# Optimization experiments

Hardware: AMD Instinct MI355X
Metric: run time of the kernel (lower is better)

## Reference

```python
import jax, jax.numpy as jnp
import numpy as np

B, W_DIM, CIN, COUT, K, H = 16, 512, 512, 512, 3, 64
PAD = (K - 1) // 2          # conv padding, also filtered_lrelu padding
GAIN = float(np.sqrt(2.0))  # lrelu gain (not torgb)
SLOPE = 0.2                 # lrelu slope (not torgb)
CLAMP = 256.0               # conv_clamp
AFFINE_WG = float(1.0 / np.sqrt(W_DIM))  # FullyConnectedLayer weight_gain


def setup_inputs() -> dict:
    key = jax.random.key(0)
    k0, k1, k2, k3 = jax.random.split(key, 4)
    return {
        "x": jax.random.normal(k0, (B, CIN, H, H), jnp.float32),
        "w": jax.random.normal(k1, (B, W_DIM), jnp.float32),
        "affine_weight": jax.random.normal(k2, (CIN, W_DIM), jnp.float32),
        "affine_bias": jnp.ones((CIN,), jnp.float32),       # bias_init=1
        "conv_weight": jax.random.normal(k3, (COUT, CIN, K, K), jnp.float32),
        "bias": jnp.zeros((COUT,), jnp.float32),
        "magnitude_ema": jnp.ones((), jnp.float32),
    }


def reference(x, w, affine_weight, affine_bias, conv_weight, bias, magnitude_ema):
    input_gain = jax.lax.rsqrt(magnitude_ema)
    # --- affine (FullyConnectedLayer, linear act, lr_mult=1) ---
    s = w @ (affine_weight * AFFINE_WG).T + affine_bias          # [B, CIN]
    # --- modulated_conv2d with demodulation (is_torgb=False) ---
    wk = conv_weight * jax.lax.rsqrt(
        jnp.mean(jnp.square(conv_weight), axis=(1, 2, 3), keepdims=True))
    s = s * jax.lax.rsqrt(jnp.mean(jnp.square(s)))
    wb = wk[None] * s[:, None, :, None, None]                    # [B,COUT,CIN,K,K]
    dcoefs = jax.lax.rsqrt(jnp.sum(jnp.square(wb), axis=(2, 3, 4)) + 1e-8)  # [B,COUT]
    wb = wb * dcoefs[:, :, None, None, None] * input_gain
    # grouped conv: groups = batch, one weight set per sample
    xg = x.reshape(1, B * CIN, H, H)
    wg = wb.reshape(B * COUT, CIN, K, K)
    y = jax.lax.conv_general_dilated(
        xg, wg, window_strides=(1, 1), padding=[(PAD, PAD), (PAD, PAD)],
        dimension_numbers=("NCHW", "OIHW", "NCHW"), feature_group_count=B)
    y = y.reshape(B, COUT, H, H)
    # --- filtered_lrelu: up=down=1, fu=fd=None (identity FIR) ---
    # => bias add, zero-pad by `padding`, lrelu * gain, clamp
    y = y + bias[:, None, None]
    y = jnp.pad(y, ((0, 0), (0, 0), (PAD, PAD), (PAD, PAD)))
    y = jnp.where(y >= 0, y, y * SLOPE) * GAIN
    y = jnp.clip(y, -CLAMP, CLAMP)                               # [B,COUT,66,66]
    return y
```

## Files before the change

kernel.cpp:

```cpp
#include <hip/hip_runtime.h>

#define B_     16
#define WDIM   512
#define CIN_   512
#define COUT_  512
#define HH     64
#define KC     32
#define NCHUNK (CIN_/KC)
#define AFFINE_WG 0.044194173824159216f
#define GAIN_  1.4142135623730951f
#define CLAMP_ 256.0f

typedef __attribute__((ext_vector_type(4))) float f32x4;
typedef __attribute__((ext_vector_type(8))) short bf16x8;
typedef __attribute__((ext_vector_type(8))) unsigned short u16x8;

__device__ __forceinline__ unsigned short f2bf(float f) {
    union { float f; unsigned u; } un; un.f = f;
    unsigned u = un.u;
    u += 0x7FFFu + ((u >> 16) & 1u);
    return (unsigned short)(u >> 16);
}

__device__ __forceinline__ void gl_lds16(const void* g, void* l) {
    __builtin_amdgcn_global_load_lds(
        reinterpret_cast<const __attribute__((address_space(1))) unsigned int*>(
            reinterpret_cast<uintptr_t>(g)),
        reinterpret_cast<__attribute__((address_space(3))) unsigned int*>(
            reinterpret_cast<uintptr_t>(l)),
        16, 0, 0);
}

__global__ void k_prepA(const float* __restrict__ w, const float* __restrict__ aw,
                        const float* __restrict__ ab, const float* __restrict__ cw,
                        float* __restrict__ s, float* __restrict__ part,
                        float* __restrict__ alpha, float* __restrict__ Q,
                        unsigned short* __restrict__ wb) {
    const int bi  = blockIdx.x;
    const int tid = threadIdx.x;
    __shared__ float redA[256];
    __shared__ float qsh[512];
    __shared__ float a_sh;
    __shared__ char tile[36864];

    if (bi < 32) {
        const int b = bi >> 1;
        const int c = ((bi & 1) << 8) + tid;
        const f32x4* wr = (const f32x4*)(w + (size_t)b * WDIM);
        const f32x4* ar = (const f32x4*)(aw + (size_t)c * WDIM);
        float acc = 0.f;
        #pragma unroll 4
        for (int k = 0; k < WDIM / 4; ++k) {
            f32x4 a = ar[k], bb = wr[k];
            acc += a[0]*bb[0] + a[1]*bb[1] + a[2]*bb[2] + a[3]*bb[3];
        }
        float sv = acc * AFFINE_WG + ab[c];
        s[b * CIN_ + c] = sv;
        redA[tid] = sv * sv;
        __syncthreads();
        for (int off = 128; off > 0; off >>= 1) {
            if (tid < off) redA[tid] += redA[tid + off];
            __syncthreads();
        }
        if (tid == 0) part[bi] = redA[0];
    } else if (bi < 544) {
        const int o = bi - 32;
        float tot = 0.f;
        #pragma unroll
        for (int half = 0; half < 2; ++half) {
            const int c = tid + half * 256;
            const float* p = cw + ((size_t)o * 512 + c) * 9;
            float qs = 0.f;
            #pragma unroll
            for (int t = 0; t < 9; ++t) { float v = p[t]; qs += v * v; }
            qsh[c] = qs; tot += qs;
        }
        redA[tid] = tot; __syncthreads();
        for (int off = 128; off > 0; off >>= 1) {
            if (tid < off) redA[tid] += redA[tid + off];
            __syncthreads();
        }
        if (tid == 0) { a_sh = rsqrtf(redA[0] * (1.0f / 4608.0f)); alpha[o] = a_sh; }
        __syncthreads();
        const float a2 = a_sh * a_sh;
        Q[(size_t)o * 512 + tid]       = a2 * qsh[tid];
        Q[(size_t)o * 512 + tid + 256] = a2 * qsh[tid + 256];
    } else {
        const int p = bi - 544;
        const int ot = p >> 4, cc = p & 15;
        const float* base = cw + ((size_t)(ot * 64) * 512 + cc * 32) * 9;
        #pragma unroll
        for (int k = 0; k < 18; ++k) {
            const int lin4 = tid + k * 256;
            const int row  = lin4 / 72;
            const int i4   = lin4 - row * 72;
            const f32x4 v = *(const f32x4*)(base + (size_t)row * 4608 + i4 * 4);
            #pragma unroll
            for (int j = 0; j < 4; ++j) {
                const int e   = i4 * 4 + j;
                const int c   = e / 9;
                const int tap = e - c * 9;
                const int byte = ((tap * 2048 + row * 32 + c) << 1) ^ ((row & 6) << 3);
                *(unsigned short*)(tile + byte) = f2bf(v[j]);
            }
        }
        __syncthreads();
        u16x8* dst = (u16x8*)(wb + (size_t)p * 18432);
        const u16x8* src = (const u16x8*)tile;
        #pragma unroll
        for (int k = 0; k < 9; ++k) dst[tid + k * 256] = src[tid + k * 256];
    }
}

__global__ void k_prepB(const float* __restrict__ x, const float* __restrict__ s,
                        const float* __restrict__ part, const float* __restrict__ Q,
                        const float* __restrict__ alpha, const float* __restrict__ ema,
                        float* __restrict__ g, unsigned short* __restrict__ xbf) {
    const int bi  = blockIdx.x;
    const int tid = threadIdx.x;
    __shared__ float rs2_sh;
    __shared__ char tile[8 * 4096];

    if (bi < 32) {
        const int b = bi >> 1;
        const int o = ((bi & 1) << 8) + tid;
        if (tid == 0) {
            float t = 0.f;
            #pragma unroll
            for (int i = 0; i < 32; ++i) t += part[i];
            rs2_sh = 8192.0f / t;
        }
        __syncthreads();
        const f32x4* sh = (const f32x4*)(s + (size_t)b * CIN_);
        const f32x4* qq = (const f32x4*)(Q + (size_t)o * CIN_);
        float d = 0.f;
        #pragma unroll 4
        for (int k = 0; k < CIN_ / 4; ++k) {
            f32x4 a = sh[k], q4 = qq[k];
            d += a[0]*a[0]*q4[0] + a[1]*a[1]*q4[1] + a[2]*a[2]*q4[2] + a[3]*a[3]*q4[3];
        }
        const float ig = rsqrtf(ema[0]);
        g[b * COUT_ + o] = alpha[o] * rsqrtf(d * rs2_sh + 1e-8f) * ig;
    } else {
        if (tid == 0) {
            float t = 0.f;
            #pragma unroll
            for (int i = 0; i < 32; ++i) t += part[i];
            rs2_sh = rsqrtf(t * (1.0f / 8192.0f));
        }
        __syncthreads();
        const float rs = rs2_sh;
        const int blk = bi - 32;
        const int b  = blk >> 7;
        const int cc = (blk >> 3) & 15;
        const int rg = blk & 7;
        const int c   = tid >> 3;
        const int k8  = tid & 7;
        const float sc = s[b * CIN_ + cc * 32 + c] * rs;
        const float* src = x + (((size_t)(b * CIN_ + cc * 32 + c)) * HH + rg * 8) * HH + k8 * 8;
        #pragma unroll
        for (int row = 0; row < 8; ++row) {
            const f32x4 v0 = *(const f32x4*)(src + (size_t)row * HH);
            const f32x4 v1 = *(const f32x4*)(src + (size_t)row * HH + 4);
            #pragma unroll
            for (int q = 0; q < 8; ++q) {
                const float v = (q < 4) ? v0[q] : v1[q - 4];
                const int col = k8 * 8 + q + 1;
                const int byte = ((col * 64 + 2 * c) ^ ((col & 6) << 3)) - 64;
                *(unsigned short*)(tile + row * 4096 + byte) = f2bf(v * sc);
            }
        }
        __syncthreads();
        unsigned short* dst = xbf + ((size_t)(b * 16 + cc) * 64 + rg * 8) * 2048;
        const u16x8* tsrc = (const u16x8*)tile;
        #pragma unroll
        for (int k = 0; k < 8; ++k)
            *(u16x8*)(dst + (size_t)(tid + k * 256) * 8) = tsrc[tid + k * 256];
    }
}

__global__ __launch_bounds__(256, 2) void k_conv2c(
    const unsigned short* __restrict__ xbf, const unsigned short* __restrict__ wb,
    const float* __restrict__ g, const float* __restrict__ bias,
    float* __restrict__ out) {
    __shared__ unsigned short Wlds[9 * 64 * 32];
    __shared__ unsigned short Xlds[6 * 66 * 32];

    const int tid  = threadIdx.x;
    const int lane = tid & 63;
    const int wv   = tid >> 6;
    const int l15  = lane & 15;
    const int hi   = lane >> 4;
    const int b  = blockIdx.z;
    const int ot = blockIdx.y;
    const int rt = blockIdx.x;
    const int h0 = rt * 4;

    const f32x4 zero4 = {0.f, 0.f, 0.f, 0.f};
    f32x4 acc[4][4];
    #pragma unroll
    for (int i = 0; i < 4; ++i)
        #pragma unroll
        for (int j = 0; j < 4; ++j) acc[i][j] = zero4;

    {
        unsigned int* p = (unsigned int*)Xlds;
        for (int i = tid; i < 6 * 66 * 32 / 2; i += 256) p[i] = 0u;
    }
    __syncthreads();

    const char* wsrc0 = (const char*)wb + (size_t)ot * 16 * 36864;
    const char* xsrc0 = (const char*)xbf + (size_t)b * 16 * 262144;

    for (int cc = 0; cc < NCHUNK; ++cc) {
        const char* wsrc = wsrc0 + (size_t)cc * 36864;
        #pragma unroll
        for (int r = 0; r < 9; ++r)
            gl_lds16(wsrc + r * 4096 + tid * 16,
                     (char*)Wlds + r * 4096 + wv * 1024);
        const char* xsrc = xsrc0 + (size_t)cc * 262144;
        #pragma unroll
        for (int r = 0; r < 6; ++r) {
            const int h_in = h0 - 1 + r;
            if ((unsigned)h_in < 64u)
                gl_lds16(xsrc + (size_t)h_in * 4096 + tid * 16,
                         (char*)Xlds + r * 4224 + 64 + wv * 1024);
        }
        __syncthreads();

        #pragma unroll
        for (int tap = 0; tap < 9; ++tap) {
            const int ti = tap / 3, tj = tap - ti * 3;
            bf16x8 af[4];
            #pragma unroll
            for (int mi = 0; mi < 4; ++mi) {
                const int o = mi * 16 + l15;
                int byte = (tap << 12) + (o << 6) + (hi << 4);
                byte ^= ((o & 6) << 3);
                af[mi] = *(const bf16x8*)((const char*)Wlds + byte);
            }
            bf16x8 bg[4];
            const int row = wv + ti;
            #pragma unroll
            for (int ni = 0; ni < 4; ++ni) {
                const int col = ni * 16 + l15 + tj;
                int byte = (((row * 66 + col) << 5) + (hi << 3)) << 1;
                byte ^= ((col & 6) << 3);
                bg[ni] = *(const bf16x8*)((const char*)Xlds + byte);
            }
            #pragma unroll
            for (int mi = 0; mi < 4; ++mi)
                #pragma unroll
                for (int ni = 0; ni < 4; ++ni)
                    acc[mi][ni] = __builtin_amdgcn_mfma_f32_16x16x32_bf16(
                        af[mi], bg[ni], acc[mi][ni], 0, 0, 0);
        }
        if (cc != NCHUNK - 1) __syncthreads();
    }

    {
        const int obase = ot * 64;
        const int orow = h0 + wv + 1;
        #pragma unroll
        for (int mi = 0; mi < 4; ++mi) {
            #pragma unroll
            for (int r = 0; r < 4; ++r) {
                const int o = obase + mi * 16 + hi * 4 + r;
                const float gg = g[b * COUT_ + o];
                const float bb = bias[o];
                float* op = out + ((size_t)(b * COUT_ + o) * 66 + orow) * 66;
                #pragma unroll
                for (int ni = 0; ni < 4; ++ni) {
                    float v = acc[mi][ni][r] * gg + bb;
                    v = (v >= 0.f ? v : v * 0.2f) * GAIN_;
                    v = fminf(fmaxf(v, -CLAMP_), CLAMP_);
                    op[ni * 16 + l15 + 1] = v;
                }
            }
        }
        #pragma unroll
        for (int k = 0; k < 2; ++k) {
            const int i = tid + k * 256;
            const int o = obase + (i >> 3);
            const int rr = (i >> 1) & 3;
            const int col = (i & 1) ? 65 : 0;
            out[((size_t)(b * COUT_ + o) * 66 + h0 + rr + 1) * 66 + col] = 0.f;
        }
        if (rt == 0 || rt == 15) {
            const int row = (rt == 0) ? 0 : 65;
            for (int i = tid; i < 64 * 66; i += 256) {
                const int o = obase + i / 66, col = i - (i / 66) * 66;
                out[((size_t)(b * COUT_ + o) * 66 + row) * 66 + col] = 0.f;
            }
        }
    }
}

extern "C" void kernel_launch(void* const* d_in, const int* in_sizes, int n_in,
                              void* d_out, int out_size, void* d_ws, size_t ws_size,
                              hipStream_t stream) {
    const float* x    = (const float*)d_in[0];
    const float* w    = (const float*)d_in[1];
    const float* aw   = (const float*)d_in[2];
    const float* ab   = (const float*)d_in[3];
    const float* cw   = (const float*)d_in[4];
    const float* bias = (const float*)d_in[5];
    const float* ema  = (const float*)d_in[6];
    float* out = (float*)d_out;

    float* wsf   = (float*)d_ws;
    float* s     = wsf;
    float* part  = wsf + 8192;
    float* alpha = wsf + 16512;
    float* Q     = wsf + 17024;
    float* g     = wsf + 279168;
    unsigned short* wb  = (unsigned short*)((char*)d_ws + 1179648);
    unsigned short* xbf = (unsigned short*)((char*)d_ws + 5898240);

    k_prepA <<<672, 256, 0, stream>>>(w, aw, ab, cw, s, part, alpha, Q, wb);
    k_prepB <<<2080, 256, 0, stream>>>(x, s, part, Q, alpha, ema, g, xbf);
    k_conv2c<<<dim3(16, 8, 16), 256, 0, stream>>>(xbf, wb, g, bias, out);
}
```

Measured before the change: 308.4 us.

## Prefetch next-tap LDS fragments and move border zeroing into prep kernel

```diff
diff --git a/kernel.cpp b/kernel.cpp
--- a/kernel.cpp
+++ b/kernel.cpp
@@ -35,7 +35,7 @@
                         const float* __restrict__ ab, const float* __restrict__ cw,
                         float* __restrict__ s, float* __restrict__ part,
                         float* __restrict__ alpha, float* __restrict__ Q,
-                        unsigned short* __restrict__ wb) {
+                        unsigned short* __restrict__ wb, float* __restrict__ out) {
     const int bi  = blockIdx.x;
     const int tid = threadIdx.x;
     __shared__ float redA[256];
@@ -85,7 +85,7 @@
         const float a2 = a_sh * a_sh;
         Q[(size_t)o * 512 + tid]       = a2 * qsh[tid];
         Q[(size_t)o * 512 + tid + 256] = a2 * qsh[tid + 256];
-    } else {
+    } else if (bi < 672) {
         const int p = bi - 544;
         const int ot = p >> 4, cc = p & 15;
         const float* base = cw + ((size_t)(ot * 64) * 512 + cc * 32) * 9;
@@ -109,6 +109,19 @@
         const u16x8* src = (const u16x8*)tile;
         #pragma unroll
         for (int k = 0; k < 9; ++k) dst[tid + k * 256] = src[tid + k * 256];
+    } else {
+        const int base = (bi - 672) * 2048;
+        #pragma unroll
+        for (int k = 0; k < 8; ++k) {
+            const int f = base + k * 256 + tid;
+            const int bo = f / 260;
+            const int r = f - bo * 260;
+            int row, col;
+            if (r < 66)       { row = 0;  col = r; }
+            else if (r < 132) { row = 65; col = r - 66; }
+            else { const int rr = r - 132; row = 1 + (rr >> 1); col = (rr & 1) ? 65 : 0; }
+            out[((size_t)bo * 66 + row) * 66 + col] = 0.f;
+        }
     }
 }
 
@@ -179,7 +192,7 @@
     }
 }
 
-__global__ __launch_bounds__(256, 2) void k_conv2c(
+__global__ __launch_bounds__(256, 2) void k_conv2d(
     const unsigned short* __restrict__ xbf, const unsigned short* __restrict__ wb,
     const float* __restrict__ g, const float* __restrict__ bias,
     float* __restrict__ out) {
@@ -212,6 +225,15 @@
     const char* wsrc0 = (const char*)wb + (size_t)ot * 16 * 36864;
     const char* xsrc0 = (const char*)xbf + (size_t)b * 16 * 262144;
 
+    int wfo[4], xco[4];
+    #pragma unroll
+    for (int mi = 0; mi < 4; ++mi) {
+        const int o = mi * 16 + l15;
+        wfo[mi] = ((o << 6) + (hi << 4)) ^ ((o & 6) << 3);
+    }
+    #pragma unroll
+    for (int ni = 0; ni < 4; ++ni) xco[ni] = ni * 16 + l15;
+
     for (int cc = 0; cc < NCHUNK; ++cc) {
         const char* wsrc = wsrc0 + (size_t)cc * 36864;
         #pragma unroll
@@ -228,32 +250,47 @@
         }
         __syncthreads();
 
+        bf16x8 afc[4], bgc[4], afn[4], bgn[4];
+        {
+            #pragma unroll
+            for (int mi = 0; mi < 4; ++mi)
+                afc[mi] = *(const bf16x8*)((const char*)Wlds + wfo[mi]);
+            const int row0 = wv;
+            #pragma unroll
+            for (int ni = 0; ni < 4; ++ni) {
+                const int col = xco[ni];
+                int byte = (((row0 * 66 + col) << 5) + (hi << 3)) << 1;
+                byte ^= ((col & 6) << 3);
+                bgc[ni] = *(const bf16x8*)((const char*)Xlds + byte);
+            }
+        }
         #pragma unroll
         for (int tap = 0; tap < 9; ++tap) {
-            const int ti = tap / 3, tj = tap - ti * 3;
-            bf16x8 af[4];
-            #pragma unroll
-            for (int mi = 0; mi < 4; ++mi) {
-                const int o = mi * 16 + l15;
-                int byte = (tap << 12) + (o << 6) + (hi << 4);
-                byte ^= ((o & 6) << 3);
-                af[mi] = *(const bf16x8*)((const char*)Wlds + byte);
-            }
-            bf16x8 bg[4];
-            const int row = wv + ti;
-            #pragma unroll
-            for (int ni = 0; ni < 4; ++ni) {
-                const int col = ni * 16 + l15 + tj;
-                int byte = (((row * 66 + col) << 5) + (hi << 3)) << 1;
-                byte ^= ((col & 6) << 3);
-                bg[ni] = *(const bf16x8*)((const char*)Xlds + byte);
-            }
+            if (tap < 8) {
+                const int tn = tap + 1;
+                const int tin = tn / 3, tjn = tn - tin * 3;
+                #pragma unroll
+                for (int mi = 0; mi < 4; ++mi)
+                    afn[mi] = *(const bf16x8*)((const char*)Wlds + (tn << 12) + wfo[mi]);
+                const int rown = wv + tin;
+                #pragma unroll
+                for (int ni = 0; ni < 4; ++ni) {
+                    const int col = xco[ni] + tjn;
+                    int byte = (((rown * 66 + col) << 5) + (hi << 3)) << 1;
+                    byte ^= ((col & 6) << 3);
+                    bgn[ni] = *(const bf16x8*)((const char*)Xlds + byte);
+                }
+            }
+            __builtin_amdgcn_s_setprio(1);
             #pragma unroll
             for (int mi = 0; mi < 4; ++mi)
                 #pragma unroll
                 for (int ni = 0; ni < 4; ++ni)
                     acc[mi][ni] = __builtin_amdgcn_mfma_f32_16x16x32_bf16(
-                        af[mi], bg[ni], acc[mi][ni], 0, 0, 0);
+                        afc[mi], bgc[ni], acc[mi][ni], 0, 0, 0);
+            __builtin_amdgcn_s_setprio(0);
+            #pragma unroll
+            for (int q = 0; q < 4; ++q) { afc[q] = afn[q]; bgc[q] = bgn[q]; }
         }
         if (cc != NCHUNK - 1) __syncthreads();
     }
@@ -278,21 +315,6 @@
                 }
             }
         }
-        #pragma unroll
-        for (int k = 0; k < 2; ++k) {
-            const int i = tid + k * 256;
-            const int o = obase + (i >> 3);
-            const int rr = (i >> 1) & 3;
-            const int col = (i & 1) ? 65 : 0;
-            out[((size_t)(b * COUT_ + o) * 66 + h0 + rr + 1) * 66 + col] = 0.f;
-        }
-        if (rt == 0 || rt == 15) {
-            const int row = (rt == 0) ? 0 : 65;
-            for (int i = tid; i < 64 * 66; i += 256) {
-                const int o = obase + i / 66, col = i - (i / 66) * 66;
-                out[((size_t)(b * COUT_ + o) * 66 + row) * 66 + col] = 0.f;
-            }
-        }
     }
 }
 
@@ -317,7 +339,7 @@
     unsigned short* wb  = (unsigned short*)((char*)d_ws + 1179648);
     unsigned short* xbf = (unsigned short*)((char*)d_ws + 5898240);
 
-    k_prepA <<<672, 256, 0, stream>>>(w, aw, ab, cw, s, part, alpha, Q, wb);
+    k_prepA <<<1712, 256, 0, stream>>>(w, aw, ab, cw, s, part, alpha, Q, wb, out);
     k_prepB <<<2080, 256, 0, stream>>>(x, s, part, Q, alpha, ema, g, xbf);
-    k_conv2c<<<dim3(16, 8, 16), 256, 0, stream>>>(xbf, wb, g, bias, out);
-}
+    k_conv2d<<<dim3(16, 8, 16), 256, 0, stream>>>(xbf, wb, g, bias, out);
+}
```

Result: no change. 310.8 us (+0.8%).

## Split weight staging in two and software-pipeline LDS fragment loads in conv

Applied to the files above, without the earlier changes.

```diff
diff --git a/kernel.cpp b/kernel.cpp
--- a/kernel.cpp
+++ b/kernel.cpp
@@ -179,11 +179,12 @@
     }
 }
 
-__global__ __launch_bounds__(256, 2) void k_conv2c(
+__global__ __launch_bounds__(256, 2) void k_conv2e(
     const unsigned short* __restrict__ xbf, const unsigned short* __restrict__ wb,
     const float* __restrict__ g, const float* __restrict__ bias,
     float* __restrict__ out) {
-    __shared__ unsigned short Wlds[9 * 64 * 32];
+    __shared__ unsigned short Wlds1[5 * 2048];
+    __shared__ unsigned short Wlds2[4 * 2048];
     __shared__ unsigned short Xlds[6 * 66 * 32];
 
     const int tid  = threadIdx.x;
@@ -212,12 +213,39 @@
     const char* wsrc0 = (const char*)wb + (size_t)ot * 16 * 36864;
     const char* xsrc0 = (const char*)xbf + (size_t)b * 16 * 262144;
 
+    int wfo[4], xco[4];
+    #pragma unroll
+    for (int mi = 0; mi < 4; ++mi) {
+        const int o = mi * 16 + l15;
+        wfo[mi] = ((o << 6) + (hi << 4)) ^ ((o & 6) << 3);
+    }
+    #pragma unroll
+    for (int ni = 0; ni < 4; ++ni) xco[ni] = ni * 16 + l15;
+
+    auto LOADW = [&](int tap, bf16x8* af) {
+        const char* base = (tap < 5) ? ((const char*)Wlds1 + (tap << 12))
+                                     : ((const char*)Wlds2 + ((tap - 5) << 12));
+        #pragma unroll
+        for (int mi = 0; mi < 4; ++mi)
+            af[mi] = *(const bf16x8*)(base + wfo[mi]);
+    };
+    auto LOADX = [&](int tap, bf16x8* bg) {
+        const int ti = tap / 3, tj = tap - ti * 3;
+        const int row = wv + ti;
+        #pragma unroll
+        for (int ni = 0; ni < 4; ++ni) {
+            const int col = xco[ni] + tj;
+            int byte = (((row * 66 + col) << 5) + (hi << 3)) << 1;
+            byte ^= ((col & 6) << 3);
+            bg[ni] = *(const bf16x8*)((const char*)Xlds + byte);
+        }
+    };
+
     for (int cc = 0; cc < NCHUNK; ++cc) {
         const char* wsrc = wsrc0 + (size_t)cc * 36864;
         #pragma unroll
-        for (int r = 0; r < 9; ++r)
-            gl_lds16(wsrc + r * 4096 + tid * 16,
-                     (char*)Wlds + r * 4096 + wv * 1024);
+        for (int r = 0; r < 5; ++r)
+            gl_lds16(wsrc + r * 4096 + tid * 16, (char*)Wlds1 + r * 4096 + tid * 16);
         const char* xsrc = xsrc0 + (size_t)cc * 262144;
         #pragma unroll
         for (int r = 0; r < 6; ++r) {
@@ -229,31 +257,45 @@
         __syncthreads();
 
         #pragma unroll
-        for (int tap = 0; tap < 9; ++tap) {
-            const int ti = tap / 3, tj = tap - ti * 3;
-            bf16x8 af[4];
-            #pragma unroll
-            for (int mi = 0; mi < 4; ++mi) {
-                const int o = mi * 16 + l15;
-                int byte = (tap << 12) + (o << 6) + (hi << 4);
-                byte ^= ((o & 6) << 3);
-                af[mi] = *(const bf16x8*)((const char*)Wlds + byte);
-            }
-            bf16x8 bg[4];
-            const int row = wv + ti;
-            #pragma unroll
-            for (int ni = 0; ni < 4; ++ni) {
-                const int col = ni * 16 + l15 + tj;
-                int byte = (((row * 66 + col) << 5) + (hi << 3)) << 1;
-                byte ^= ((col & 6) << 3);
-                bg[ni] = *(const bf16x8*)((const char*)Xlds + byte);
-            }
+        for (int r = 5; r < 9; ++r)
+            gl_lds16(wsrc + r * 4096 + tid * 16, (char*)Wlds2 + (r - 5) * 4096 + tid * 16);
+
+        bf16x8 afc[4], bgc[4], afn[4], bgn[4];
+        LOADW(0, afc); LOADX(0, bgc);
+        #pragma unroll
+        for (int tap = 0; tap < 5; ++tap) {
+            if (tap < 4) { LOADW(tap + 1, afn); LOADX(tap + 1, bgn); }
+            __builtin_amdgcn_s_setprio(1);
             #pragma unroll
             for (int mi = 0; mi < 4; ++mi)
                 #pragma unroll
                 for (int ni = 0; ni < 4; ++ni)
                     acc[mi][ni] = __builtin_amdgcn_mfma_f32_16x16x32_bf16(
-                        af[mi], bg[ni], acc[mi][ni], 0, 0, 0);
+                        afc[mi], bgc[ni], acc[mi][ni], 0, 0, 0);
+            __builtin_amdgcn_s_setprio(0);
+            if (tap < 4) {
+                #pragma unroll
+                for (int q = 0; q < 4; ++q) { afc[q] = afn[q]; bgc[q] = bgn[q]; }
+            }
+        }
+        __syncthreads();
+
+        LOADW(5, afc); LOADX(5, bgc);
+        #pragma unroll
+        for (int tap = 5; tap < 9; ++tap) {
+            if (tap < 8) { LOADW(tap + 1, afn); LOADX(tap + 1, bgn); }
+            __builtin_amdgcn_s_setprio(1);
+            #pragma unroll
+            for (int mi = 0; mi < 4; ++mi)
+                #pragma unroll
+                for (int ni = 0; ni < 4; ++ni)
+                    acc[mi][ni] = __builtin_amdgcn_mfma_f32_16x16x32_bf16(
+                        afc[mi], bgc[ni], acc[mi][ni], 0, 0, 0);
+            __builtin_amdgcn_s_setprio(0);
+            if (tap < 8) {
+                #pragma unroll
+                for (int q = 0; q < 4; ++q) { afc[q] = afn[q]; bgc[q] = bgn[q]; }
+            }
         }
         if (cc != NCHUNK - 1) __syncthreads();
     }
@@ -319,5 +361,5 @@
 
     k_prepA <<<672, 256, 0, stream>>>(w, aw, ab, cw, s, part, alpha, Q, wb);
     k_prepB <<<2080, 256, 0, stream>>>(x, s, part, Q, alpha, ema, g, xbf);
-    k_conv2c<<<dim3(16, 8, 16), 256, 0, stream>>>(xbf, wb, g, bias, out);
-}
+    k_conv2e<<<dim3(16, 8, 16), 256, 0, stream>>>(xbf, wb, g, bias, out);
+}
```

Measured after the change: 306.0 us. Within noise of the previous version (-0.8%).
